# Kernel optimization log

Measured on AMD Instinct MI355X. Metric: run time of the kernel, lower is better.

## Reference

```python
import jax, jax.numpy as jnp
import numpy as np

N_NODES = 50000
N_EDGES = 800000
IN_DIM = 256
OUT_DIM = 32
HEADS = 4
NEG_SLOPE = 0.2  # PyG GATConv default
LN_EPS = 1e-5


def setup_inputs() -> dict:
    key = jax.random.key(0)
    ks = jax.random.split(key, 8)
    x = jax.random.normal(ks[0], (N_NODES, IN_DIM), dtype=jnp.float32)
    edge_index = jax.random.randint(ks[1], (2, N_EDGES), 0, N_NODES, dtype=jnp.int64)
    # Glorot-ish scaling for stability
    W = jax.random.normal(ks[2], (IN_DIM, HEADS * OUT_DIM), dtype=jnp.float32) / np.sqrt(IN_DIM)
    att_src = jax.random.normal(ks[3], (HEADS, OUT_DIM), dtype=jnp.float32) / np.sqrt(OUT_DIM)
    att_dst = jax.random.normal(ks[4], (HEADS, OUT_DIM), dtype=jnp.float32) / np.sqrt(OUT_DIM)
    bias = jax.random.normal(ks[5], (HEADS * OUT_DIM,), dtype=jnp.float32) * 0.02
    gamma = jnp.ones((HEADS * OUT_DIM,), dtype=jnp.float32)
    beta = jnp.zeros((HEADS * OUT_DIM,), dtype=jnp.float32)
    return {"x": x, "edge_index": edge_index, "W": W, "att_src": att_src,
            "att_dst": att_dst, "bias": bias, "gamma": gamma, "beta": beta}


def reference(x, edge_index, W, att_src, att_dst, bias, gamma, beta):
    N = x.shape[0]
    H, C = att_src.shape
    # --- GATConv (PyG semantics, eval mode so attention dropout is identity) ---
    # add self-loops (PyG default add_self_loops=True)
    loops = jnp.arange(N, dtype=edge_index.dtype)
    src = jnp.concatenate([edge_index[0], loops])  # [E+N]
    dst = jnp.concatenate([edge_index[1], loops])
    h = (x @ W).reshape(N, H, C)                    # [N,H,C] (lin has no bias)
    a_s = jnp.einsum('nhc,hc->nh', h, att_src)      # [N,H]
    a_d = jnp.einsum('nhc,hc->nh', h, att_dst)
    e = jax.nn.leaky_relu(a_s[src] + a_d[dst], NEG_SLOPE)  # [E+N,H]
    # segment softmax over incoming edges of each destination node
    emax = jax.ops.segment_max(e, dst, num_segments=N)     # every node has a self-loop
    ee = jnp.exp(e - emax[dst])
    denom = jax.ops.segment_sum(ee, dst, num_segments=N)
    alpha = ee / denom[dst]                                 # [E+N,H]
    msg = h[src] * alpha[:, :, None]                        # [E+N,H,C]
    out = jax.ops.segment_sum(msg, dst, num_segments=N).reshape(N, H * C) + bias
    # --- LayerNorm ---
    mu = out.mean(-1, keepdims=True)
    var = ((out - mu) ** 2).mean(-1, keepdims=True)
    out = (out - mu) * jax.lax.rsqrt(var + LN_EPS) * gamma + beta
    # --- dropout (eval: identity) + ELU ---
    return jax.nn.elu(out)
```

## Files before the change

kernel.cpp:

```cpp
#include <hip/hip_runtime.h>
#include <hip/hip_bf16.h>
#include <cstdint>
#include <cstddef>

#define N_NODES 50000
#define N_EDGES 800000
#define IN_DIM 256
#define HC 128
#define HEADS 4
#define NEG_SLOPE 0.2f
#define LN_EPS 1e-5f

#define POISON_I ((int)0xAAAAAAAAu)

#define NGB ((N_NODES + 63) / 64)
#define CAP 64

typedef _Float16 f16x8 __attribute__((ext_vector_type(8)));
typedef _Float16 f16x2 __attribute__((ext_vector_type(2)));
typedef float f32x4 __attribute__((ext_vector_type(4)));

__device__ __forceinline__ float lrelu(float x) { return x > 0.f ? x : NEG_SLOPE * x; }
__device__ __forceinline__ unsigned pack_h2(float a, float b) {
    f16x2 h; h[0] = (_Float16)a; h[1] = (_Float16)b;
    return *(unsigned*)&h;
}

__global__ __launch_bounds__(256) void k_fused(
    const float* __restrict__ x, const float* __restrict__ W,
    const int* __restrict__ ei,
    const float* __restrict__ att_src, const float* __restrict__ att_dst,
    _Float16* __restrict__ h16, float* __restrict__ a_s, float* __restrict__ a_d,
    int* __restrict__ counts, int* __restrict__ rec)
{
    __shared__ _Float16 Wlds[32768];
    const int tid = threadIdx.x;
    const int b = blockIdx.x;

    if (b & 1) {
        const int eb = (b >> 1) << 10;
#pragma unroll
        for (int it = 0; it < 4; ++it) {
            int e = eb + it * 256 + tid;
            if (e < N_EDGES) {
                int dst = ei[N_EDGES + e];
                int r = atomicAdd(&counts[dst], 1) - POISON_I;
                rec[(dst << 6) + r] = ei[e];
            }
        }
        return;
    }

    const int gb   = b >> 1;
    const int wave = tid >> 6;
    const int lane = tid & 63;
    const int col  = lane & 15;
    const int quad = lane >> 4;
    const int m0   = gb * 64 + wave * 16;

    const int rowA = min(m0 + col, N_NODES - 1);
    const float* xrow = x + (size_t)rowA * IN_DIM + quad * 8;

    float4 xr[16];
#pragma unroll
    for (int kt = 0; kt < 8; ++kt) {
        xr[2 * kt]     = *(const float4*)(xrow + kt * 32);
        xr[2 * kt + 1] = *(const float4*)(xrow + kt * 32 + 4);
    }

    {
#pragma unroll
        for (int it = 0; it < 16; ++it) {
            int c = it * 256 + tid;
            int ccol = c & 15, cquad = (c >> 4) & 3, cnt = (c >> 6) & 7, ckt = c >> 9;
            const float* wp = W + (size_t)(ckt * 32 + cquad * 8) * HC + cnt * 16 + ccol;
            f16x8 v;
#pragma unroll
            for (int j = 0; j < 8; ++j) v[j] = (_Float16)wp[j * HC];
            *(f16x8*)(Wlds + (size_t)c * 8) = v;
        }
    }
    __syncthreads();

    f32x4 acc[8];
#pragma unroll
    for (int nt = 0; nt < 8; ++nt) acc[nt] = (f32x4){0.f, 0.f, 0.f, 0.f};

#pragma unroll
    for (int kt = 0; kt < 8; ++kt) {
        float4 xa = xr[2 * kt], xb = xr[2 * kt + 1];
        f16x8 a;
        a[0] = (_Float16)xa.x; a[1] = (_Float16)xa.y;
        a[2] = (_Float16)xa.z; a[3] = (_Float16)xa.w;
        a[4] = (_Float16)xb.x; a[5] = (_Float16)xb.y;
        a[6] = (_Float16)xb.z; a[7] = (_Float16)xb.w;
#pragma unroll
        for (int nt = 0; nt < 8; ++nt) {
            f16x8 bb = *(const f16x8*)&Wlds[((kt * 8 + nt) * 64 + quad * 16 + col) * 8];
            acc[nt] = __builtin_amdgcn_mfma_f32_16x16x32_f16(a, bb, acc[nt], 0, 0, 0);
        }
    }

    f16x2* h2g = (f16x2*)h16;
#pragma unroll
    for (int a2 = 0; a2 < 4; ++a2) {
#pragma unroll
        for (int r = 0; r < 4; ++r) {
            int row = m0 + quad * 4 + r;
            if (row < N_NODES) {
                f16x2 hv;
                hv[0] = (_Float16)acc[2 * a2][r];
                hv[1] = (_Float16)acc[2 * a2 + 1][r];
                h2g[(size_t)row * 64 + a2 * 16 + col] = hv;
            }
        }
    }

    float pS[4][4], pD[4][4];
#pragma unroll
    for (int hd = 0; hd < 4; ++hd)
#pragma unroll
        for (int r = 0; r < 4; ++r) { pS[hd][r] = 0.f; pD[hd][r] = 0.f; }

#pragma unroll
    for (int nt = 0; nt < 8; ++nt) {
        int ch = nt * 16 + col;
        float sv = att_src[ch], dv = att_dst[ch];
        int hd = nt >> 1;
#pragma unroll
        for (int r = 0; r < 4; ++r) {
            pS[hd][r] += acc[nt][r] * sv;
            pD[hd][r] += acc[nt][r] * dv;
        }
    }
#pragma unroll
    for (int off = 1; off < 16; off <<= 1) {
#pragma unroll
        for (int hd = 0; hd < 4; ++hd)
#pragma unroll
            for (int r = 0; r < 4; ++r) {
                pS[hd][r] += __shfl_xor(pS[hd][r], off, 16);
                pD[hd][r] += __shfl_xor(pD[hd][r], off, 16);
            }
    }
    if (col == 0) {
#pragma unroll
        for (int r = 0; r < 4; ++r) {
            int row = m0 + quad * 4 + r;
            if (row < N_NODES) {
#pragma unroll
                for (int hd = 0; hd < 4; ++hd) {
                    a_s[row * HEADS + hd] = pS[hd][r];
                    a_d[row * HEADS + hd] = pD[hd][r];
                }
            }
        }
    }
}

__global__ __launch_bounds__(256) void k_gather(
    const int* __restrict__ counts, const int* __restrict__ rec,
    const float* __restrict__ a_s, const float* __restrict__ a_d,
    const _Float16* __restrict__ h16, const float* __restrict__ bias,
    const float* __restrict__ gamma, const float* __restrict__ beta,
    float* __restrict__ out)
{
    __shared__ int   lsrc[256];
    __shared__ uint2 lw[256];

    int gid = blockIdx.x * 256 + threadIdx.x;
    int n = gid >> 6, lane = gid & 63;
    if (n >= N_NODES) return;

    const int wbase = (threadIdx.x >> 6) * 64;
    const int beg = n << 6;
    const int deg = counts[n] - POISON_I;
    const int hd = lane >> 4;
    const f16x2* h2 = (const f16x2*)h16;
    const unsigned short* lwh = (const unsigned short*)&lw[wbase];

    const float4 ad4 = *(const float4*)(a_d + (size_t)n * HEADS);
    const float adh = (hd == 0) ? ad4.x : (hd == 1) ? ad4.y : (hd == 2) ? ad4.z : ad4.w;
    const float wSelf = __expf(lrelu(a_s[n * HEADS + hd] + adh));
    float den = wSelf;
    f16x2 hv = h2[(size_t)n * 64 + lane];
    float acc0 = (float)hv[0] * wSelf;
    float acc1 = (float)hv[1] * wSelf;

    for (int base = 0; base < deg; base += 64) {
        int nc = min(64, deg - base);
        if (lane < nc) {
            int src = rec[beg + base + lane];
            lsrc[wbase + lane] = src;
            float4 s4 = *(const float4*)(a_s + (size_t)src * HEADS);
            float w0 = __expf(lrelu(s4.x + ad4.x));
            float w1 = __expf(lrelu(s4.y + ad4.y));
            float w2 = __expf(lrelu(s4.z + ad4.z));
            float w3 = __expf(lrelu(s4.w + ad4.w));
            lw[wbase + lane] = (uint2){pack_h2(w0, w1), pack_h2(w2, w3)};
        }
        int j = 0;
        for (; j + 8 <= nc; j += 8) {
            int s[8]; float w[8]; f16x2 hh[8];
#pragma unroll
            for (int k = 0; k < 8; ++k) {
                s[k] = lsrc[wbase + j + k];
                unsigned short uw = lwh[(j + k) * 4 + hd];
                _Float16 wf = *(_Float16*)&uw;
                w[k] = (float)wf;
            }
#pragma unroll
            for (int k = 0; k < 8; ++k) hh[k] = h2[(size_t)s[k] * 64 + lane];
#pragma unroll
            for (int k = 0; k < 8; ++k) {
                acc0 += (float)hh[k][0] * w[k];
                acc1 += (float)hh[k][1] * w[k];
                den  += w[k];
            }
        }
        for (; j < nc; ++j) {
            int s0 = lsrc[wbase + j];
            unsigned short uw = lwh[j * 4 + hd];
            _Float16 wf = *(_Float16*)&uw;
            float w0 = (float)wf;
            f16x2 hx = h2[(size_t)s0 * 64 + lane];
            acc0 += (float)hx[0] * w0;
            acc1 += (float)hx[1] * w0;
            den  += w0;
        }
    }

    const int c0 = (lane >> 4) * 32 + (lane & 15);
    const int c1 = c0 + 16;
    float v0 = acc0 / den + bias[c0];
    float v1 = acc1 / den + bias[c1];
    float s = v0 + v1;
#pragma unroll
    for (int off = 32; off; off >>= 1) s += __shfl_xor(s, off, 64);
    float mu = s * (1.f / 128.f);
    float d0 = v0 - mu, d1 = v1 - mu;
    float q = d0 * d0 + d1 * d1;
#pragma unroll
    for (int off = 32; off; off >>= 1) q += __shfl_xor(q, off, 64);
    float rs = rsqrtf(q * (1.f / 128.f) + LN_EPS);
    float o0 = d0 * rs * gamma[c0] + beta[c0];
    float o1 = d1 * rs * gamma[c1] + beta[c1];
    o0 = o0 > 0.f ? o0 : __expf(o0) - 1.f;
    o1 = o1 > 0.f ? o1 : __expf(o1) - 1.f;
    out[(size_t)n * HC + c0] = o0;
    out[(size_t)n * HC + c1] = o1;
}

extern "C" void kernel_launch(void* const* d_in, const int* in_sizes, int n_in,
                              void* d_out, int out_size, void* d_ws, size_t ws_size,
                              hipStream_t stream) {
    const float* x       = (const float*)d_in[0];
    const int*   ei      = (const int*)d_in[1];
    const float* W       = (const float*)d_in[2];
    const float* att_src = (const float*)d_in[3];
    const float* att_dst = (const float*)d_in[4];
    const float* bias    = (const float*)d_in[5];
    const float* gamma   = (const float*)d_in[6];
    const float* beta    = (const float*)d_in[7];
    float* out = (float*)d_out;

    char* ws = (char*)d_ws;
    _Float16* h16    = (_Float16*)(ws);
    float*    a_s    = (float*)(ws + 12800000);
    float*    a_d    = (float*)(ws + 13600000);
    int*      rec    = (int*)  (ws + 14400000);
    int*      counts = (int*)  (ws + 27200000);

    k_fused<<<2 * NGB, 256, 0, stream>>>(x, W, ei, att_src, att_dst,
                                         h16, a_s, a_d, counts, rec);
    k_gather<<<(N_NODES * 64 + 255) / 256, 256, 0, stream>>>(
        counts, rec, a_s, a_d, h16, bias, gamma, beta, out);
}
```

Baseline: 182.2 us.

## Two-level bucketed CSR build with LDS atomics and deeper gather unroll

Replaces the per-edge global atomic scatter into per-destination slots with a two-pass scheme. Edges are first binned by dst>>8 into 196 coarse buckets using LDS counters and one global atomic per bucket per block. A new k_bucket kernel then places edges into per-node slots using LDS atomics and writes exact counts. This is meant to cut contended global atomics and scattered writes, at the cost of an extra kernel launch and an intermediate buffer. The gather loop also gains a 16-wide unrolled stage to keep more loads in flight.

```diff
diff --git a/kernel.cpp b/kernel.cpp
--- a/kernel.cpp
+++ b/kernel.cpp
@@ -15,6 +15,8 @@
 
 #define NGB ((N_NODES + 63) / 64)
 #define CAP 64
+#define NBUCK 196
+#define BSTRIDE 5120
 
 typedef _Float16 f16x8 __attribute__((ext_vector_type(8)));
 typedef _Float16 f16x2 __attribute__((ext_vector_type(2)));
@@ -31,21 +33,41 @@
     const int* __restrict__ ei,
     const float* __restrict__ att_src, const float* __restrict__ att_dst,
     _Float16* __restrict__ h16, float* __restrict__ a_s, float* __restrict__ a_d,
-    int* __restrict__ counts, int* __restrict__ rec)
+    int* __restrict__ gfill, int2* __restrict__ bucket)
 {
     __shared__ _Float16 Wlds[32768];
     const int tid = threadIdx.x;
     const int b = blockIdx.x;
 
     if (b & 1) {
+        int* cnt  = (int*)Wlds;
+        int* base = cnt + 256;
         const int eb = (b >> 1) << 10;
+        if (tid < NBUCK) cnt[tid] = 0;
+        __syncthreads();
+        int src[4], dst[4], rk[4], bk[4];
+        bool valid[4];
 #pragma unroll
         for (int it = 0; it < 4; ++it) {
             int e = eb + it * 256 + tid;
-            if (e < N_EDGES) {
-                int dst = ei[N_EDGES + e];
-                int r = atomicAdd(&counts[dst], 1) - POISON_I;
-                rec[(dst << 6) + r] = ei[e];
+            valid[it] = (e < N_EDGES);
+            src[it] = 0; dst[it] = 0; bk[it] = 0; rk[it] = 0;
+            if (valid[it]) {
+                src[it] = ei[e];
+                dst[it] = ei[N_EDGES + e];
+                bk[it]  = dst[it] >> 8;
+                rk[it]  = atomicAdd(&cnt[bk[it]], 1);
+            }
+        }
+        __syncthreads();
+        if (tid < NBUCK)
+            base[tid] = atomicAdd(&gfill[tid], cnt[tid]) - POISON_I;
+        __syncthreads();
+#pragma unroll
+        for (int it = 0; it < 4; ++it) {
+            if (valid[it]) {
+                int p = bk[it] * BSTRIDE + base[bk[it]] + rk[it];
+                bucket[p] = (int2){src[it], dst[it]};
             }
         }
         return;
@@ -72,8 +94,8 @@
 #pragma unroll
         for (int it = 0; it < 16; ++it) {
             int c = it * 256 + tid;
-            int ccol = c & 15, cquad = (c >> 4) & 3, cnt = (c >> 6) & 7, ckt = c >> 9;
-            const float* wp = W + (size_t)(ckt * 32 + cquad * 8) * HC + cnt * 16 + ccol;
+            int ccol = c & 15, cquad = (c >> 4) & 3, cnt_ = (c >> 6) & 7, ckt = c >> 9;
+            const float* wp = W + (size_t)(ckt * 32 + cquad * 8) * HC + cnt_ * 16 + ccol;
             f16x8 v;
 #pragma unroll
             for (int j = 0; j < 8; ++j) v[j] = (_Float16)wp[j * HC];
@@ -156,6 +178,26 @@
             }
         }
     }
+}
+
+__global__ __launch_bounds__(256) void k_bucket(
+    const int2* __restrict__ bucket, const int* __restrict__ gfill,
+    int* __restrict__ rec, int* __restrict__ counts)
+{
+    __shared__ int cnt[256];
+    const int b = blockIdx.x, tid = threadIdx.x;
+    cnt[tid] = 0;
+    __syncthreads();
+    const int m = gfill[b] - POISON_I;
+    const int2* bp = bucket + (size_t)b * BSTRIDE;
+    for (int i = tid; i < m; i += 256) {
+        int2 ed = bp[i];
+        int r = atomicAdd(&cnt[ed.y & 255], 1);
+        rec[((size_t)ed.y << 6) + r] = ed.x;
+    }
+    __syncthreads();
+    int n = (b << 8) + tid;
+    if (n < N_NODES) counts[n] = cnt[tid];
 }
 
 __global__ __launch_bounds__(256) void k_gather(
@@ -174,7 +216,7 @@
 
     const int wbase = (threadIdx.x >> 6) * 64;
     const int beg = n << 6;
-    const int deg = counts[n] - POISON_I;
+    const int deg = counts[n];
     const int hd = lane >> 4;
     const f16x2* h2 = (const f16x2*)h16;
     const unsigned short* lwh = (const unsigned short*)&lw[wbase];
@@ -200,22 +242,36 @@
             lw[wbase + lane] = (uint2){pack_h2(w0, w1), pack_h2(w2, w3)};
         }
         int j = 0;
-        for (; j + 8 <= nc; j += 8) {
-            int s[8]; float w[8]; f16x2 hh[8];
-#pragma unroll
-            for (int k = 0; k < 8; ++k) {
-                s[k] = lsrc[wbase + j + k];
+        for (; j + 16 <= nc; j += 16) {
+            int s[16]; f16x2 hh[16];
+#pragma unroll
+            for (int k = 0; k < 16; ++k) s[k] = lsrc[wbase + j + k];
+#pragma unroll
+            for (int k = 0; k < 16; ++k) hh[k] = h2[(size_t)s[k] * 64 + lane];
+#pragma unroll
+            for (int k = 0; k < 16; ++k) {
                 unsigned short uw = lwh[(j + k) * 4 + hd];
                 _Float16 wf = *(_Float16*)&uw;
-                w[k] = (float)wf;
-            }
+                float w = (float)wf;
+                acc0 += (float)hh[k][0] * w;
+                acc1 += (float)hh[k][1] * w;
+                den  += w;
+            }
+        }
+        for (; j + 8 <= nc; j += 8) {
+            int s[8]; f16x2 hh[8];
+#pragma unroll
+            for (int k = 0; k < 8; ++k) s[k] = lsrc[wbase + j + k];
 #pragma unroll
             for (int k = 0; k < 8; ++k) hh[k] = h2[(size_t)s[k] * 64 + lane];
 #pragma unroll
             for (int k = 0; k < 8; ++k) {
-                acc0 += (float)hh[k][0] * w[k];
-                acc1 += (float)hh[k][1] * w[k];
-                den  += w[k];
+                unsigned short uw = lwh[(j + k) * 4 + hd];
+                _Float16 wf = *(_Float16*)&uw;
+                float w = (float)wf;
+                acc0 += (float)hh[k][0] * w;
+                acc1 += (float)hh[k][1] * w;
+                den  += w;
             }
         }
         for (; j < nc; ++j) {
@@ -270,9 +326,12 @@
     float*    a_d    = (float*)(ws + 13600000);
     int*      rec    = (int*)  (ws + 14400000);
     int*      counts = (int*)  (ws + 27200000);
+    int*      gfill  = (int*)  (ws + 27400000);
+    int2*     bucket = (int2*) (ws + 27401216);
 
     k_fused<<<2 * NGB, 256, 0, stream>>>(x, W, ei, att_src, att_dst,
-                                         h16, a_s, a_d, counts, rec);
+                                         h16, a_s, a_d, gfill, bucket);
+    k_bucket<<<NBUCK, 256, 0, stream>>>(bucket, gfill, rec, counts);
     k_gather<<<(N_NODES * 64 + 255) / 256, 256, 0, stream>>>(
         counts, rec, a_s, a_d, h16, bias, gamma, beta, out);
 }
```

Result: slower. 193.2 us (+6.0%).
